# Kernel tuning notes

Hardware: AMD Instinct MI355X
Metric: run time of the kernel (lower is better)

## Reference

```python
import jax, jax.numpy as jnp
import numpy as np

N, DIN, H, E, S = 20000, 128, 2048, 2048, 2000
TPM = 0.1        # HP.TIME_PENALTY_MIXING
ENT = 0.01       # HP.ENTROPY_COEF
NEG = -1e30      # finite mask value (avoids -inf NaNs in grads)


def setup_inputs() -> dict:
    key = jax.random.key(0)
    ks = jax.random.split(key, 7)
    feature_vecs = jax.random.normal(ks[0], (N, DIN), dtype=jnp.float32)
    W1 = jax.random.normal(ks[1], (DIN, H), dtype=jnp.float32) * (1.0 / np.sqrt(DIN))
    b1 = jnp.zeros((H,), dtype=jnp.float32)
    W2 = jax.random.normal(ks[2], (H, E), dtype=jnp.float32) * (1.0 / np.sqrt(H))
    b2 = jnp.zeros((E,), dtype=jnp.float32)
    key_vec = jax.random.normal(ks[3], (E,), dtype=jnp.float32) * (1.0 / np.sqrt(E))
    rng = np.random.default_rng(0)
    mask_np = rng.random((S, N)) < 0.4           # passive-set membership per SEL event
    mask_np[:, :2] = True                        # guarantee |passive| >= 2
    good_np = rng.random(N) < 0.05               # proof_flas membership
    r = rng.random((S, N)) * mask_np
    sel_idx_np = r.argmax(axis=1)                # selected clause is inside passive set
    times_np = rng.random(S).astype(np.float32)
    return {
        "feature_vecs": feature_vecs, "W1": W1, "b1": b1, "W2": W2, "b2": b2,
        "key_vec": key_vec,
        "times": jnp.asarray(times_np),
        "mask": jnp.asarray(mask_np),
        "good": jnp.asarray(good_np),
        "sel_idx": jnp.asarray(sel_idx_np, dtype=jnp.int32),
    }


def reference(feature_vecs, W1, b1, W2, b2, key_vec, times, mask, good, sel_idx):
    # clause_embedder: 2-layer MLP; clause_key: dot with key vector -> logits [N]
    h = jax.nn.relu(feature_vecs @ W1 + b1)
    embeddings = h @ W2 + b2                     # [N, E]
    logits = embeddings @ key_vec                # [N]

    # masked log-softmax per SEL event over the passive set
    ml = jnp.where(mask, logits[None, :], NEG)   # [S, N]
    lsm = jax.nn.log_softmax(ml, axis=1)         # [S, N]

    # good-action reward loss (LEARN_FROM_ALL_GOOD)
    gm = mask & good[None, :]                    # good clauses currently passive
    ng = gm.sum(axis=1)                          # [S]
    good_terms = -jnp.where(gm, lsm, 0.0).sum(axis=1)
    has_good = ng > 0
    good_loss = jnp.sum(jnp.where(has_good, good_terms / jnp.maximum(ng, 1), 0.0))
    num_good_steps = has_good.sum()

    # time penalty loss on the selected clause's log-prob
    sel_lsm = jnp.take_along_axis(lsm, sel_idx[:, None], axis=1)[:, 0]
    time_loss = TPM * jnp.sum(times * sel_lsm)
    time_volume = jnp.sum(times)

    # normalized entropy loss
    p = jnp.exp(lsm)
    psz = mask.sum(axis=1).astype(lsm.dtype)
    minus_ent = jnp.where(mask, p * lsm, 0.0).sum(axis=1) / jnp.log(psz)
    entropy_loss = ENT * jnp.sum(minus_ent)
    num_steps = jnp.asarray(S, dtype=jnp.int32)

    return (good_loss, num_good_steps, time_loss, time_volume, entropy_loss, num_steps)
```

## Files before the change

### kernel.cpp

```cpp
#include <hip/hip_runtime.h>

#define NCL 20000
#define DIN 128
#define HID 2048
#define SEVN 2000
#define TPM 0.1f
#define ENTC 0.01f

#define RG 79
#define NJOBS (SEVN * RG)
#define LASTJOB (NJOBS - 1)
#define SPAD 2048

#define WS_B2K   0
#define WS_W2K   256
#define WS_LOGIT 8448
#define WS_CDATA 89600
#define WS_BSTG  409600
#define WS_PACK  933888
#define WS_PART  5989888

#define NB_PACK 2048
#define NB_SB   128
#define NB_WK   513

typedef __attribute__((ext_vector_type(8))) short short8;
typedef __attribute__((ext_vector_type(4))) float f32x4;

static __device__ __forceinline__ unsigned short f2bf(float f) {
    unsigned u = __float_as_uint(f);
    u += 0x7FFFu + ((u >> 16) & 1u);
    return (unsigned short)(u >> 16);
}
static __device__ __forceinline__ unsigned pck(unsigned short a, unsigned short b) {
    return (unsigned)a | ((unsigned)b << 16);
}

__global__ __launch_bounds__(256) void k_stream(const unsigned* __restrict__ mask,
                                                unsigned* __restrict__ packed,
                                                const float* __restrict__ W1,
                                                unsigned short* __restrict__ bst,
                                                const float* __restrict__ W2,
                                                const float* __restrict__ b2,
                                                const float* __restrict__ key,
                                                float* __restrict__ w2k,
                                                float* __restrict__ b2k) {
    int b = blockIdx.x;
    int t = threadIdx.x;

    if (b < NB_PACK) {
        int lane = t & 63;
        int wv   = b * 4 + (t >> 6);
        for (int job = wv; job < NJOBS; job += NB_PACK * 4) {
            int s  = job / RG;
            int gr = job - s * RG;
            const unsigned* gp = mask + (size_t)s * NCL + gr * 256;
            int off = 4 * lane;
            if (job == LASTJOB && lane >= 8) off = 0;
            uint4 m = *(const uint4*)(gp + off);
            unsigned long long B0 = __ballot(m.x != 0);
            unsigned long long B1 = __ballot(m.y != 0);
            unsigned long long B2 = __ballot(m.z != 0);
            unsigned long long B3 = __ballot(m.w != 0);
            if (lane < 8) {
                int k = lane >> 1;
                unsigned long long Bk = (k == 0) ? B0 : (k == 1) ? B1 : (k == 2) ? B2 : B3;
                unsigned v = (lane & 1) ? (unsigned)(Bk >> 32) : (unsigned)Bk;
                packed[(size_t)job * 8 + lane] = v;
            }
        }
        return;
    }
    b -= NB_PACK;

    if (b < NB_SB) {
        int g = b * 256 + t;
        int l = g & 63, c = (g >> 6) & 3, ct = g >> 8;
        int col = ct * 16 + (l & 15);
        int kb  = c * 32 + (l >> 4) * 8;
        unsigned short v[8];
        #pragma unroll
        for (int j = 0; j < 8; ++j) v[j] = f2bf(W1[(size_t)(kb + j) * HID + col]);
        uint4 o;
        o.x = pck(v[0], v[1]); o.y = pck(v[2], v[3]);
        o.z = pck(v[4], v[5]); o.w = pck(v[6], v[7]);
        ((uint4*)bst)[g] = o;
        return;
    }
    b -= NB_SB;

    {
        int wid  = b * 4 + (t >> 6);
        int lane = t & 63;
        const float4* key4 = (const float4*)key;
        float acc = 0.f;
        if (wid <= HID) {
            const float4* row4 = (const float4*)((wid < HID) ? (W2 + (size_t)wid * 2048) : b2);
            #pragma unroll
            for (int it = 0; it < 8; ++it) {
                int idx = it * 64 + lane;
                float4 a = row4[idx], k4 = key4[idx];
                acc += a.x * k4.x + a.y * k4.y + a.z * k4.z + a.w * k4.w;
            }
        }
        #pragma unroll
        for (int m = 1; m < 64; m <<= 1) acc += __shfl_xor(acc, m);
        if (lane == 0 && wid < HID) w2k[wid] = acc;
        if (lane == 0 && wid == HID) *b2k = acc;
    }
}

__global__ __launch_bounds__(256) void k_gemm(const float* __restrict__ fv,
                                              const unsigned short* __restrict__ bst,
                                              const float* __restrict__ b1,
                                              const float* __restrict__ w2k,
                                              const float* __restrict__ b2k,
                                              const int* __restrict__ good,
                                              float* __restrict__ logits,
                                              float4* __restrict__ cd) {
    int blk = blockIdx.x;
    int tid = threadIdx.x;
    int w = tid >> 6, l = tid & 63;
    int colg = l & 15, kg = l >> 4;
    int r0 = blk * 32;

    const short8* B8 = (const short8*)bst;

    short8 afrag[2][4];
    #pragma unroll
    for (int s = 0; s < 2; ++s) {
        const float* rp = fv + (size_t)(r0 + s * 16 + (l & 15)) * DIN + kg * 8;
        #pragma unroll
        for (int c = 0; c < 4; ++c) {
            float4 f0 = *(const float4*)(rp + c * 32);
            float4 f1 = *(const float4*)(rp + c * 32 + 4);
            union { short8 sv; uint4 u; } tmp;
            tmp.u.x = pck(f2bf(f0.x), f2bf(f0.y));
            tmp.u.y = pck(f2bf(f0.z), f2bf(f0.w));
            tmp.u.z = pck(f2bf(f1.x), f2bf(f1.y));
            tmp.u.w = pck(f2bf(f1.z), f2bf(f1.w));
            afrag[s][c] = tmp.sv;
        }
    }

    float acc[2][4];
    #pragma unroll
    for (int s = 0; s < 2; ++s)
        #pragma unroll
        for (int r = 0; r < 4; ++r) acc[s][r] = 0.f;

    int ct0 = w * 32;
    for (int t = 0; t < 32; ++t) {
        int ct = ct0 + t;
        short8 bfr[4];
        #pragma unroll
        for (int c = 0; c < 4; ++c) bfr[c] = B8[((ct * 4 + c) << 6) + l];
        int col = ct * 16 + colg;
        float b1v = b1[col];
        float wkv = w2k[col];
        #pragma unroll
        for (int s = 0; s < 2; ++s) {
            f32x4 d = {0.f, 0.f, 0.f, 0.f};
            #pragma unroll
            for (int c = 0; c < 4; ++c)
                d = __builtin_amdgcn_mfma_f32_16x16x32_bf16(afrag[s][c], bfr[c], d, 0, 0, 0);
            #pragma unroll
            for (int r = 0; r < 4; ++r) {
                float h = d[r] + b1v;
                h = h > 0.f ? h : 0.f;
                acc[s][r] += h * wkv;
            }
        }
    }

    __shared__ float red[4][32];
    #pragma unroll
    for (int s = 0; s < 2; ++s) {
        #pragma unroll
        for (int r = 0; r < 4; ++r) {
            float a = acc[s][r];
            a += __shfl_xor(a, 1);
            a += __shfl_xor(a, 2);
            a += __shfl_xor(a, 4);
            a += __shfl_xor(a, 8);
            if (colg == 0) red[w][s * 16 + kg * 4 + r] = a;
        }
    }
    __syncthreads();
    if (tid < 32) {
        float sum = *b2k;
        #pragma unroll
        for (int ww = 0; ww < 4; ++ww) sum += red[ww][tid];
        int row = r0 + tid;
        logits[row] = sum;
        float e = expf(sum);
        bool g = good[row] != 0;
        cd[row] = make_float4(e, e * sum, g ? sum : 0.f, g ? 1.f : 0.f);
    }
}

__global__ __launch_bounds__(256) void k_events(const unsigned* __restrict__ packed,
                                                const float4* __restrict__ cd,
                                                float* __restrict__ part) {
    int gr = blockIdx.x >> 3;
    int eg = blockIdx.x & 7;
    int s  = eg * 256 + threadIdx.x;
    float Z = 0.f, X = 0.f, cnt = 0.f, ng = 0.f, sg = 0.f;
    if (s < SEVN) {
        const unsigned* wp = packed + ((size_t)s * RG + gr) * 8;
        unsigned wv[8];
        #pragma unroll
        for (int j = 0; j < 8; ++j) wv[j] = wp[j];
        int cbase = gr * 256;
        if (gr < RG - 1) {
            #pragma unroll
            for (int k = 0; k < 4; ++k) {
                #pragma unroll
                for (int half = 0; half < 2; ++half) {
                    unsigned word = wv[2 * k + half];
                    int cb = cbase + 128 * half + k;
                    #pragma unroll
                    for (int b = 0; b < 32; ++b) {
                        float4 c = cd[cb + 4 * b];
                        float m = (float)((word >> b) & 1u);
                        Z   += m * c.x;
                        X   += m * c.y;
                        sg  += m * c.z;
                        ng  += m * c.w;
                        cnt += m;
                    }
                }
            }
        } else {
            #pragma unroll
            for (int k = 0; k < 4; ++k) {
                unsigned word = wv[2 * k];
                int cb = cbase + k;
                #pragma unroll
                for (int b = 0; b < 8; ++b) {
                    float4 c = cd[cb + 4 * b];
                    float m = (float)((word >> b) & 1u);
                    Z   += m * c.x;
                    X   += m * c.y;
                    sg  += m * c.z;
                    ng  += m * c.w;
                    cnt += m;
                }
            }
        }
    }
    float* pp = part + (size_t)gr * 5 * SPAD;
    pp[0 * SPAD + s] = Z;
    pp[1 * SPAD + s] = X;
    pp[2 * SPAD + s] = cnt;
    pp[3 * SPAD + s] = ng;
    pp[4 * SPAD + s] = sg;
}

__global__ __launch_bounds__(256) void k_final(const float* __restrict__ part,
                                               const float* __restrict__ logits,
                                               const float* __restrict__ times,
                                               const int* __restrict__ sel,
                                               float* __restrict__ out) {
    int s = blockIdx.x * 256 + threadIdx.x;
    bool live = s < SEVN;
    float Z = 0.f, X = 0.f, cnt = 0.f, ng = 0.f, sg = 0.f;
    if (live) {
        for (int c = 0; c < RG; ++c) {
            const float* pp = part + (size_t)c * 5 * SPAD;
            Z   += pp[0 * SPAD + s];
            X   += pp[1 * SPAD + s];
            cnt += pp[2 * SPAD + s];
            ng  += pp[3 * SPAD + s];
            sg  += pp[4 * SPAD + s];
        }
    }
    float gl = 0.f, ngs = 0.f, tl = 0.f, tv = 0.f, en = 0.f;
    if (live) {
        float L = logf(Z);
        if (ng > 0.5f) { gl = L - sg / ng; ngs = 1.f; }
        float tm = times[s];
        tl = TPM * tm * (logits[sel[s]] - L);
        tv = tm;
        en = ENTC * ((X / Z - L) / logf(cnt));
    }
    #pragma unroll
    for (int m = 1; m < 64; m <<= 1) {
        gl  += __shfl_xor(gl, m);
        ngs += __shfl_xor(ngs, m);
        tl  += __shfl_xor(tl, m);
        tv  += __shfl_xor(tv, m);
        en  += __shfl_xor(en, m);
    }
    if ((threadIdx.x & 63) == 0) {
        atomicAdd(out + 0, gl);
        atomicAdd(out + 1, ngs);
        atomicAdd(out + 2, tl);
        atomicAdd(out + 3, tv);
        atomicAdd(out + 4, en);
    }
    if (s == 0) out[5] = (float)SEVN;
}

extern "C" void kernel_launch(void* const* d_in, const int* in_sizes, int n_in,
                              void* d_out, int out_size, void* d_ws, size_t ws_size,
                              hipStream_t stream) {
    const float* fv    = (const float*)d_in[0];
    const float* W1    = (const float*)d_in[1];
    const float* b1    = (const float*)d_in[2];
    const float* W2    = (const float*)d_in[3];
    const float* b2    = (const float*)d_in[4];
    const float* key   = (const float*)d_in[5];
    const float* times = (const float*)d_in[6];
    const unsigned* mask = (const unsigned*)d_in[7];
    const int* good    = (const int*)d_in[8];
    const int* sel     = (const int*)d_in[9];
    float* out = (float*)d_out;
    char* ws = (char*)d_ws;

    float* w2k    = (float*)(ws + WS_W2K);
    float* b2k    = (float*)(ws + WS_B2K);
    float* logits = (float*)(ws + WS_LOGIT);
    float4* cdata = (float4*)(ws + WS_CDATA);
    unsigned short* bst = (unsigned short*)(ws + WS_BSTG);
    unsigned* packed = (unsigned*)(ws + WS_PACK);
    float* part   = (float*)(ws + WS_PART);

    hipMemsetAsync(d_out, 0, 6 * sizeof(float), stream);
    k_stream<<<NB_PACK + NB_SB + NB_WK, 256, 0, stream>>>(
        mask, packed, W1, bst, W2, b2, key, w2k, b2k);
    k_gemm <<<NCL / 32, 256, 0, stream>>>(fv, bst, b1, w2k, b2k, good, logits, cdata);
    k_events<<<RG * 8, 256, 0, stream>>>(packed, cdata, part);
    k_final<<<SPAD / 256, 256, 0, stream>>>(part, logits, times, sel, out);
}
```

Measured before the change: 358.3 us.

## Read mask directly in events kernel with per-half LDS-cached clause data

Removes the separate mask bit-packing pass. k_events now reads the 160MB int mask once and directly, with each block caching half of the per-clause exp(logit), a bf16 logit and packed good bits in LDS, then handling 8 events per block. This avoids writing and re-reading the packed mask and the float4 clause data, but stores logits as bf16 for the X and good-sum terms, which loses precision. The partials are also cut from 79 chunks to 8.

```diff
diff --git a/kernel.cpp b/kernel.cpp
--- a/kernel.cpp
+++ b/kernel.cpp
@@ -7,22 +7,22 @@
 #define TPM 0.1f
 #define ENTC 0.01f
 
-#define RG 79
-#define NJOBS (SEVN * RG)
-#define LASTJOB (NJOBS - 1)
+#define HHALF 10000
+#define EPB 8
 #define SPAD 2048
 
 #define WS_B2K   0
 #define WS_W2K   256
 #define WS_LOGIT 8448
-#define WS_CDATA 89600
-#define WS_BSTG  409600
-#define WS_PACK  933888
-#define WS_PART  5989888
-
-#define NB_PACK 2048
-#define NB_SB   128
-#define NB_WK   513
+#define WS_EARR  88576
+#define WS_LBF   168704
+#define WS_GBW   208896
+#define WS_PART  211712
+#define WS_BSTG  539648
+
+#define NB_SB 128
+#define NB_WK 513
+#define NB_GB 3
 
 typedef __attribute__((ext_vector_type(8))) short short8;
 typedef __attribute__((ext_vector_type(4))) float f32x4;
@@ -36,42 +36,17 @@
     return (unsigned)a | ((unsigned)b << 16);
 }
 
-__global__ __launch_bounds__(256) void k_stream(const unsigned* __restrict__ mask,
-                                                unsigned* __restrict__ packed,
-                                                const float* __restrict__ W1,
+__global__ __launch_bounds__(256) void k_stream(const float* __restrict__ W1,
                                                 unsigned short* __restrict__ bst,
                                                 const float* __restrict__ W2,
                                                 const float* __restrict__ b2,
                                                 const float* __restrict__ key,
+                                                const int* __restrict__ good,
                                                 float* __restrict__ w2k,
-                                                float* __restrict__ b2k) {
+                                                float* __restrict__ b2k,
+                                                unsigned* __restrict__ gbw) {
     int b = blockIdx.x;
     int t = threadIdx.x;
-
-    if (b < NB_PACK) {
-        int lane = t & 63;
-        int wv   = b * 4 + (t >> 6);
-        for (int job = wv; job < NJOBS; job += NB_PACK * 4) {
-            int s  = job / RG;
-            int gr = job - s * RG;
-            const unsigned* gp = mask + (size_t)s * NCL + gr * 256;
-            int off = 4 * lane;
-            if (job == LASTJOB && lane >= 8) off = 0;
-            uint4 m = *(const uint4*)(gp + off);
-            unsigned long long B0 = __ballot(m.x != 0);
-            unsigned long long B1 = __ballot(m.y != 0);
-            unsigned long long B2 = __ballot(m.z != 0);
-            unsigned long long B3 = __ballot(m.w != 0);
-            if (lane < 8) {
-                int k = lane >> 1;
-                unsigned long long Bk = (k == 0) ? B0 : (k == 1) ? B1 : (k == 2) ? B2 : B3;
-                unsigned v = (lane & 1) ? (unsigned)(Bk >> 32) : (unsigned)Bk;
-                packed[(size_t)job * 8 + lane] = v;
-            }
-        }
-        return;
-    }
-    b -= NB_PACK;
 
     if (b < NB_SB) {
         int g = b * 256 + t;
@@ -89,7 +64,7 @@
     }
     b -= NB_SB;
 
-    {
+    if (b < NB_WK) {
         int wid  = b * 4 + (t >> 6);
         int lane = t & 63;
         const float4* key4 = (const float4*)key;
@@ -107,6 +82,21 @@
         for (int m = 1; m < 64; m <<= 1) acc += __shfl_xor(acc, m);
         if (lane == 0 && wid < HID) w2k[wid] = acc;
         if (lane == 0 && wid == HID) *b2k = acc;
+        return;
+    }
+    b -= NB_WK;
+
+    {
+        int id = b * 256 + t;
+        if (id < 626) {
+            int h = id / 313, w = id - h * 313;
+            int base = h * HHALF + 32 * w;
+            int nb = (w == 312) ? 16 : 32;
+            unsigned wordv = 0;
+            for (int j = 0; j < nb; ++j)
+                wordv |= (good[base + j] != 0 ? 1u : 0u) << j;
+            gbw[h * 320 + w] = wordv;
+        }
     }
 }
 
@@ -115,9 +105,9 @@
                                               const float* __restrict__ b1,
                                               const float* __restrict__ w2k,
                                               const float* __restrict__ b2k,
-                                              const int* __restrict__ good,
                                               float* __restrict__ logits,
-                                              float4* __restrict__ cd) {
+                                              float* __restrict__ Earr,
+                                              unsigned short* __restrict__ Lbf) {
     int blk = blockIdx.x;
     int tid = threadIdx.x;
     int w = tid >> 6, l = tid & 63;
@@ -193,68 +183,105 @@
         for (int ww = 0; ww < 4; ++ww) sum += red[ww][tid];
         int row = r0 + tid;
         logits[row] = sum;
-        float e = expf(sum);
-        bool g = good[row] != 0;
-        cd[row] = make_float4(e, e * sum, g ? sum : 0.f, g ? 1.f : 0.f);
-    }
-}
-
-__global__ __launch_bounds__(256) void k_events(const unsigned* __restrict__ packed,
-                                                const float4* __restrict__ cd,
+        Earr[row] = expf(sum);
+        Lbf[row]  = f2bf(sum);
+    }
+}
+
+__global__ __launch_bounds__(256) void k_events(const unsigned* __restrict__ mask,
+                                                const float* __restrict__ Earr,
+                                                const unsigned short* __restrict__ Lbf,
+                                                const unsigned* __restrict__ gbw,
                                                 float* __restrict__ part) {
-    int gr = blockIdx.x >> 3;
-    int eg = blockIdx.x & 7;
-    int s  = eg * 256 + threadIdx.x;
-    float Z = 0.f, X = 0.f, cnt = 0.f, ng = 0.f, sg = 0.f;
-    if (s < SEVN) {
-        const unsigned* wp = packed + ((size_t)s * RG + gr) * 8;
-        unsigned wv[8];
-        #pragma unroll
-        for (int j = 0; j < 8; ++j) wv[j] = wp[j];
-        int cbase = gr * 256;
-        if (gr < RG - 1) {
-            #pragma unroll
-            for (int k = 0; k < 4; ++k) {
-                #pragma unroll
-                for (int half = 0; half < 2; ++half) {
-                    unsigned word = wv[2 * k + half];
-                    int cb = cbase + 128 * half + k;
-                    #pragma unroll
-                    for (int b = 0; b < 32; ++b) {
-                        float4 c = cd[cb + 4 * b];
-                        float m = (float)((word >> b) & 1u);
-                        Z   += m * c.x;
-                        X   += m * c.y;
-                        sg  += m * c.z;
-                        ng  += m * c.w;
-                        cnt += m;
-                    }
-                }
+    __shared__ float Es[HHALF];
+    __shared__ unsigned short Ls[HHALF];
+    __shared__ unsigned Gs[313];
+    int blk = blockIdx.x;
+    int h  = blk & 1;
+    int eg = blk >> 1;
+    int t = threadIdx.x;
+
+    {
+        const float4* Eg4 = (const float4*)(Earr + h * HHALF);
+        float4* Es4 = (float4*)Es;
+        #pragma unroll
+        for (int j = 0; j < 10; ++j) {
+            int idx = j * 256 + t;
+            if (idx < 2500) Es4[idx] = Eg4[idx];
+        }
+        const uint4* Lg4 = (const uint4*)(Lbf + h * HHALF);
+        uint4* Ls4 = (uint4*)Ls;
+        #pragma unroll
+        for (int j = 0; j < 5; ++j) {
+            int idx = j * 256 + t;
+            if (idx < 1250) Ls4[idx] = Lg4[idx];
+        }
+        if (t < 313) Gs[t] = gbw[h * 320 + t];
+        int t2 = t + 256;
+        if (t2 < 313) Gs[t2] = gbw[h * 320 + t2];
+    }
+    __syncthreads();
+
+    int wv = t >> 6, lane = t & 63;
+    int shiftbit = t & 31;
+    float* pc = part + (size_t)(h * 4 + wv) * 5 * SPAD;
+
+    for (int e = 0; e < EPB; ++e) {
+        int s = eg * EPB + e;
+        const unsigned* mrow = mask + (size_t)s * NCL + h * HHALF;
+        float Z = 0.f, X = 0.f, cnt = 0.f, ng = 0.f, sg = 0.f;
+        for (int kb = 0; kb < 3; ++kb) {
+            unsigned mv[13];
+            #pragma unroll
+            for (int j = 0; j < 13; ++j)
+                mv[j] = mrow[(kb * 13 + j) * 256 + t];
+            #pragma unroll
+            for (int j = 0; j < 13; ++j) {
+                int i = (kb * 13 + j) * 256 + t;
+                float E = Es[i];
+                float l = __uint_as_float(((unsigned)Ls[i]) << 16);
+                unsigned gw = Gs[i >> 5];
+                bool m = mv[j] != 0u;
+                bool g = ((gw >> shiftbit) & 1u) != 0u;
+                float me = m ? E : 0.f;
+                Z += me;
+                X = fmaf(me, l, X);
+                cnt += m ? 1.f : 0.f;
+                sg += (m && g) ? l : 0.f;
+                ng += (m && g) ? 1.f : 0.f;
             }
-        } else {
-            #pragma unroll
-            for (int k = 0; k < 4; ++k) {
-                unsigned word = wv[2 * k];
-                int cb = cbase + k;
-                #pragma unroll
-                for (int b = 0; b < 8; ++b) {
-                    float4 c = cd[cb + 4 * b];
-                    float m = (float)((word >> b) & 1u);
-                    Z   += m * c.x;
-                    X   += m * c.y;
-                    sg  += m * c.z;
-                    ng  += m * c.w;
-                    cnt += m;
-                }
-            }
-        }
-    }
-    float* pp = part + (size_t)gr * 5 * SPAD;
-    pp[0 * SPAD + s] = Z;
-    pp[1 * SPAD + s] = X;
-    pp[2 * SPAD + s] = cnt;
-    pp[3 * SPAD + s] = ng;
-    pp[4 * SPAD + s] = sg;
+        }
+        if (t < 16) {
+            int i = 9984 + t;
+            unsigned mvt = mrow[i];
+            float E = Es[i];
+            float l = __uint_as_float(((unsigned)Ls[i]) << 16);
+            unsigned gw = Gs[i >> 5];
+            bool m = mvt != 0u;
+            bool g = ((gw >> (i & 31)) & 1u) != 0u;
+            float me = m ? E : 0.f;
+            Z += me;
+            X = fmaf(me, l, X);
+            cnt += m ? 1.f : 0.f;
+            sg += (m && g) ? l : 0.f;
+            ng += (m && g) ? 1.f : 0.f;
+        }
+        #pragma unroll
+        for (int m = 1; m < 64; m <<= 1) {
+            Z   += __shfl_xor(Z, m);
+            X   += __shfl_xor(X, m);
+            cnt += __shfl_xor(cnt, m);
+            ng  += __shfl_xor(ng, m);
+            sg  += __shfl_xor(sg, m);
+        }
+        if (lane == 0) {
+            pc[0 * SPAD + s] = Z;
+            pc[1 * SPAD + s] = X;
+            pc[2 * SPAD + s] = cnt;
+            pc[3 * SPAD + s] = ng;
+            pc[4 * SPAD + s] = sg;
+        }
+    }
 }
 
 __global__ __launch_bounds__(256) void k_final(const float* __restrict__ part,
@@ -266,7 +293,8 @@
     bool live = s < SEVN;
     float Z = 0.f, X = 0.f, cnt = 0.f, ng = 0.f, sg = 0.f;
     if (live) {
-        for (int c = 0; c < RG; ++c) {
+        #pragma unroll
+        for (int c = 0; c < 8; ++c) {
             const float* pp = part + (size_t)c * 5 * SPAD;
             Z   += pp[0 * SPAD + s];
             X   += pp[1 * SPAD + s];
@@ -321,15 +349,16 @@
     float* w2k    = (float*)(ws + WS_W2K);
     float* b2k    = (float*)(ws + WS_B2K);
     float* logits = (float*)(ws + WS_LOGIT);
-    float4* cdata = (float4*)(ws + WS_CDATA);
+    float* Earr   = (float*)(ws + WS_EARR);
+    unsigned short* Lbf = (unsigned short*)(ws + WS_LBF);
+    unsigned* gbw = (unsigned*)(ws + WS_GBW);
+    float* part   = (float*)(ws + WS_PART);
     unsigned short* bst = (unsigned short*)(ws + WS_BSTG);
-    unsigned* packed = (unsigned*)(ws + WS_PACK);
-    float* part   = (float*)(ws + WS_PART);
 
     hipMemsetAsync(d_out, 0, 6 * sizeof(float), stream);
-    k_stream<<<NB_PACK + NB_SB + NB_WK, 256, 0, stream>>>(
-        mask, packed, W1, bst, W2, b2, key, w2k, b2k);
-    k_gemm <<<NCL / 32, 256, 0, stream>>>(fv, bst, b1, w2k, b2k, good, logits, cdata);
-    k_events<<<RG * 8, 256, 0, stream>>>(packed, cdata, part);
+    k_stream<<<NB_SB + NB_WK + NB_GB, 256, 0, stream>>>(W1, bst, W2, b2, key, good,
+                                                        w2k, b2k, gbw);
+    k_gemm <<<NCL / 32, 256, 0, stream>>>(fv, bst, b1, w2k, b2k, logits, Earr, Lbf);
+    k_events<<<500, 256, 0, stream>>>(mask, Earr, Lbf, gbw, part);
     k_final<<<SPAD / 256, 256, 0, stream>>>(part, logits, times, sel, out);
 }
```

After: 303.6 us. -15.3%, faster.
